# Kernel optimization log

Hardware: AMD Instinct MI355X
Metric: run time of the kernel (lower is better)

The kernel has to match this reference:

```python
import jax, jax.numpy as jnp
import numpy as np

N = 50000      # nodes
E = 800000     # edges (avg degree 16)
F_IN = 128     # in_channels
F_OUT = 64     # out_channels per head
H = 8          # attn heads
ALPHA = 0.2    # leaky relu slope


def setup_inputs() -> dict:
    key = jax.random.key(0)
    k1, k2, k3, k4, k5 = jax.random.split(key, 5)
    x = jax.random.normal(k1, (N, F_IN), dtype=jnp.float32)
    # guarantee every row appears as a source so rowsum > 0 (avoids NaN div)
    src = jnp.concatenate([jnp.arange(N, dtype=jnp.int32),
                           jax.random.randint(k2, (E - N,), 0, N, dtype=jnp.int32)])
    dst = jax.random.randint(k3, (E,), 0, N, dtype=jnp.int32)
    edge = jnp.stack([src, dst])  # [2, E]
    glorot = (6.0 / (F_IN + F_OUT)) ** 0.5
    W = jax.random.uniform(k4, (H, F_IN, F_OUT), jnp.float32, -glorot, glorot)
    a = jax.random.normal(k5, (H, 2 * F_OUT), dtype=jnp.float32) * 0.05
    return {"x": x, "edge": edge, "W": W, "a": a}


def reference(x, edge, W, a):
    # dropout p=0.6 treated in eval mode (identity); activation=None -> identity
    n = x.shape[0]
    src, dst = edge[0], edge[1]
    # per-head projected features: [H, N, F_OUT]
    h = jnp.einsum('nf,hfo->hno', x, W)
    a_src, a_dst = a[:, :F_OUT], a[:, F_OUT:]
    # edge scores a . cat(h_src, h_dst) decomposed into two node-level dots
    s = (jnp.einsum('hno,ho->hn', h, a_src)[:, src]
         + jnp.einsum('hno,ho->hn', h, a_dst)[:, dst])          # [H, E]
    edge_e = jnp.exp(-jax.nn.leaky_relu(s, ALPHA))               # [H, E]
    seg = lambda v: jax.ops.segment_sum(v, src, num_segments=n)
    rowsum = jax.vmap(seg)(edge_e)                               # [H, N] == spmm(e, ones)
    msg = edge_e[..., None] * h[:, dst, :]                       # [H, E, F_OUT]
    h_prime = jax.vmap(seg)(msg)                                 # [H, N, F_OUT]
    out = h_prime / rowsum[..., None]
    # concat heads: [N, H*F_OUT]
    return jnp.transpose(out, (1, 0, 2)).reshape(n, H * F_OUT)
```

## Files before the change

kernel.cpp:

```cpp
#include <hip/hip_runtime.h>
#include <hip/hip_bf16.h>
#include <math.h>

#define N_NODES 50000
#define N_EDGES 800000
#define FIN 128
#define FOUT 64
#define NH 8
#define ALPHA 0.2f
#define HSTRIDE (NH * FOUT)
#define SCAN_B 196

#define X2BF_B 3125
#define BPT_B  64
#define APERM_B 4
#define HIST_B 1563
#define PREP_B (X2BF_B + BPT_B + APERM_B + HIST_B)

typedef __attribute__((ext_vector_type(8))) short bf16x8;
typedef __attribute__((ext_vector_type(4))) float f32x4;

__device__ __forceinline__ unsigned pack_bf2(float lo, float hi) {
    __hip_bfloat162 b = __float22bfloat162_rn(make_float2(lo, hi));
    return *(unsigned*)&b;
}

__global__ __launch_bounds__(256) void gat_prep(const float* __restrict__ x,
                                                const float* __restrict__ W,
                                                const float* __restrict__ a,
                                                const int* __restrict__ src,
                                                unsigned* __restrict__ xbf,
                                                unsigned* __restrict__ bpt,
                                                float* __restrict__ aperm,
                                                int* __restrict__ deg) {
    const int b = blockIdx.x;
    const int t = threadIdx.x;

    if (b < X2BF_B) {
        const size_t tt = (size_t)b * 256 + t;
        const size_t i  = tt * 8;
        const float4 v0 = *(const float4*)(x + i);
        const float4 v1 = *(const float4*)(x + i + 4);
        uint4 o;
        o.x = pack_bf2(v0.x, v0.y);
        o.y = pack_bf2(v0.z, v0.w);
        o.z = pack_bf2(v1.x, v1.y);
        o.w = pack_bf2(v1.z, v1.w);
        *(uint4*)(xbf + tt * 4) = o;
    } else if (b < X2BF_B + BPT_B) {
        const int gt   = (b - X2BF_B) * 256 + t;
        const int dcol = gt >> 5;
        const int kq   = gt & 31;
        const int head = dcol & 7, col = dcol >> 3;
        const float* wp = W + (size_t)head * (FIN * FOUT) + (size_t)(kq * 4) * FOUT + col;
        uint2 pk;
        pk.x = pack_bf2(wp[0],        wp[FOUT]);
        pk.y = pack_bf2(wp[2 * FOUT], wp[3 * FOUT]);
        *(uint2*)(bpt + (size_t)dcol * (FIN / 2) + kq * 2) = pk;
    } else if (b < X2BF_B + BPT_B + APERM_B) {
        const int idx  = (b - X2BF_B - BPT_B) * 256 + t;
        const int tab  = idx >> 9;
        const int dcol = idx & 511;
        aperm[idx] = a[(dcol & 7) * (2 * FOUT) + tab * FOUT + (dcol >> 3)];
    } else {
        const int e = ((b - X2BF_B - BPT_B - APERM_B) * 256 + t) * 2;
        if (e + 1 < N_EDGES) {
            const int2 s2 = *(const int2*)(src + e);
            atomicAdd(&deg[s2.x], 1);
            atomicAdd(&deg[s2.y], 1);
        } else if (e < N_EDGES) {
            atomicAdd(&deg[src[e]], 1);
        }
    }
}

__global__ __launch_bounds__(256) void gat_proj(const unsigned short* __restrict__ xbf,
                                                const unsigned short* __restrict__ bpt,
                                                const float* __restrict__ aperm,
                                                unsigned short* __restrict__ h2,
                                                float* __restrict__ ssrc,
                                                float* __restrict__ sdst) {
    const int lane = threadIdx.x & 63;
    const int wid  = blockIdx.x * 4 + (threadIdx.x >> 6);
    const int m0   = wid * 32;
    const int l15  = lane & 15;
    const int g    = lane >> 4;

    bf16x8 xf[2][4];
#pragma unroll
    for (int nh = 0; nh < 2; ++nh) {
        int node = m0 + nh * 16 + l15;
        if (node > N_NODES - 1) node = N_NODES - 1;
        const unsigned short* p = xbf + (size_t)node * FIN + g * 8;
#pragma unroll
        for (int ks = 0; ks < 4; ++ks)
            xf[nh][ks] = *(const bf16x8*)(p + ks * 32);
    }

    float sc1[2][4], sc2[2][4];
#pragma unroll
    for (int nh = 0; nh < 2; ++nh)
#pragma unroll
        for (int r = 0; r < 4; ++r) { sc1[nh][r] = 0.f; sc2[nh][r] = 0.f; }

    for (int stp = 0; stp < 16; ++stp) {
        const int dc0 = stp * 32;
        f32x4 acc[2][2];
#pragma unroll
        for (int dh = 0; dh < 2; ++dh)
#pragma unroll
            for (int nh = 0; nh < 2; ++nh)
                acc[dh][nh] = (f32x4){0.f, 0.f, 0.f, 0.f};

#pragma unroll
        for (int dh = 0; dh < 2; ++dh) {
            const unsigned short* p = bpt + (size_t)(dc0 + dh * 16 + l15) * FIN + g * 8;
#pragma unroll
            for (int ks = 0; ks < 4; ++ks) {
                const bf16x8 af = *(const bf16x8*)(p + ks * 32);
                acc[dh][0] = __builtin_amdgcn_mfma_f32_16x16x32_bf16(af, xf[0][ks], acc[dh][0], 0, 0, 0);
                acc[dh][1] = __builtin_amdgcn_mfma_f32_16x16x32_bf16(af, xf[1][ks], acc[dh][1], 0, 0, 0);
            }
        }

#pragma unroll
        for (int dh = 0; dh < 2; ++dh) {
            const float4 ap1 = *(const float4*)&aperm[dc0 + dh * 16 + g * 4];
            const float4 ap2 = *(const float4*)&aperm[512 + dc0 + dh * 16 + g * 4];
#pragma unroll
            for (int nh = 0; nh < 2; ++nh) {
                sc1[nh][0] += acc[dh][nh][0] * ap1.x;  sc2[nh][0] += acc[dh][nh][0] * ap2.x;
                sc1[nh][1] += acc[dh][nh][1] * ap1.y;  sc2[nh][1] += acc[dh][nh][1] * ap2.y;
                sc1[nh][2] += acc[dh][nh][2] * ap1.z;  sc2[nh][2] += acc[dh][nh][2] * ap2.z;
                sc1[nh][3] += acc[dh][nh][3] * ap1.w;  sc2[nh][3] += acc[dh][nh][3] * ap2.w;
            }
        }

#pragma unroll
        for (int nh = 0; nh < 2; ++nh) {
            const int node = m0 + nh * 16 + l15;
            if (node < N_NODES) {
#pragma unroll
                for (int dh = 0; dh < 2; ++dh) {
                    const int dc = dc0 + dh * 16 + g * 4;
                    uint2 pk;
                    pk.x = pack_bf2(acc[dh][nh][0], acc[dh][nh][1]);
                    pk.y = pack_bf2(acc[dh][nh][2], acc[dh][nh][3]);
                    *(uint2*)((char*)h2 + ((size_t)node * HSTRIDE + dc) * 2) = pk;
                }
            }
        }
    }

#pragma unroll
    for (int nh = 0; nh < 2; ++nh) {
        const int node = m0 + nh * 16 + l15;
        float4 v1 = make_float4(sc1[nh][0], sc1[nh][1], sc1[nh][2], sc1[nh][3]);
        float4 v2 = make_float4(sc2[nh][0], sc2[nh][1], sc2[nh][2], sc2[nh][3]);
        v1.x += __shfl_xor(v1.x, 32, 64); v1.y += __shfl_xor(v1.y, 32, 64);
        v1.z += __shfl_xor(v1.z, 32, 64); v1.w += __shfl_xor(v1.w, 32, 64);
        v2.x += __shfl_xor(v2.x, 32, 64); v2.y += __shfl_xor(v2.y, 32, 64);
        v2.z += __shfl_xor(v2.z, 32, 64); v2.w += __shfl_xor(v2.w, 32, 64);
        if (node < N_NODES) {
            if (g == 0) { *(float4*)&ssrc[node * 8]     = v1; *(float4*)&sdst[node * 8]     = v2; }
            if (g == 1) { *(float4*)&ssrc[node * 8 + 4] = v1; *(float4*)&sdst[node * 8 + 4] = v2; }
        }
    }
}

__global__ __launch_bounds__(256) void scan_bsum(const int* __restrict__ deg,
                                                 int* __restrict__ bsum) {
    __shared__ int sm[256];
    const int t   = threadIdx.x;
    const int gid = blockIdx.x * 256 + t;
    sm[t] = (gid < N_NODES) ? deg[gid] : 0;
    __syncthreads();
#pragma unroll
    for (int off = 128; off > 0; off >>= 1) {
        if (t < off) sm[t] += sm[t + off];
        __syncthreads();
    }
    if (t == 0) bsum[blockIdx.x] = sm[0];
}

__global__ __launch_bounds__(256) void scan_part(int* __restrict__ bsum) {
    __shared__ int sm[256];
    const int t = threadIdx.x;
    const int v = (t < SCAN_B) ? bsum[t] : 0;
    sm[t] = v;
    __syncthreads();
    for (int off = 1; off < 256; off <<= 1) {
        const int u = (t >= off) ? sm[t - off] : 0;
        __syncthreads();
        sm[t] += u;
        __syncthreads();
    }
    if (t < SCAN_B) bsum[t] = sm[t] - v;
}

__global__ __launch_bounds__(256) void scan_write(const int* __restrict__ deg,
                                                  const int* __restrict__ bsum,
                                                  int* __restrict__ row_start,
                                                  int* __restrict__ cursor) {
    __shared__ int sm[256];
    const int t   = threadIdx.x;
    const int gid = blockIdx.x * 256 + t;
    const int v   = (gid < N_NODES) ? deg[gid] : 0;
    sm[t] = v;
    __syncthreads();
    for (int off = 1; off < 256; off <<= 1) {
        const int u = (t >= off) ? sm[t - off] : 0;
        __syncthreads();
        sm[t] += u;
        __syncthreads();
    }
    if (gid < N_NODES) {
        const int rs = bsum[blockIdx.x] + sm[t] - v;
        row_start[gid] = rs;
        cursor[gid]    = rs;
    }
    if (blockIdx.x == 0 && t == 0) row_start[N_NODES] = N_EDGES;
}

__global__ __launch_bounds__(256) void gat_fill(const int* __restrict__ src,
                                                const int* __restrict__ dst,
                                                int* __restrict__ cursor,
                                                int* __restrict__ csr_dst) {
    const int e = blockIdx.x * 256 + threadIdx.x;
    if (e >= N_EDGES) return;
    const int pos = atomicAdd(&cursor[src[e]], 1);
    csr_dst[pos] = dst[e];
}

#define GAT_LD(KK) (*(const uint4*)(h2b + ((size_t)(unsigned)__builtin_amdgcn_readlane(d, (KK)) << 10) + lofs))

#define GAT_FMA(HV, KK) do {                                                          \
    const float e0 = __int_as_float(__builtin_amdgcn_readlane(__float_as_int(e[0]), (KK))); \
    const float e1 = __int_as_float(__builtin_amdgcn_readlane(__float_as_int(e[1]), (KK))); \
    const float e2 = __int_as_float(__builtin_amdgcn_readlane(__float_as_int(e[2]), (KK))); \
    const float e3 = __int_as_float(__builtin_amdgcn_readlane(__float_as_int(e[3]), (KK))); \
    const float e4 = __int_as_float(__builtin_amdgcn_readlane(__float_as_int(e[4]), (KK))); \
    const float e5 = __int_as_float(__builtin_amdgcn_readlane(__float_as_int(e[5]), (KK))); \
    const float e6 = __int_as_float(__builtin_amdgcn_readlane(__float_as_int(e[6]), (KK))); \
    const float e7 = __int_as_float(__builtin_amdgcn_readlane(__float_as_int(e[7]), (KK))); \
    acc[0] += e0 * __int_as_float((HV).x << 16);                                      \
    acc[1] += e1 * __int_as_float((HV).x & 0xFFFF0000u);                              \
    acc[2] += e2 * __int_as_float((HV).y << 16);                                      \
    acc[3] += e3 * __int_as_float((HV).y & 0xFFFF0000u);                              \
    acc[4] += e4 * __int_as_float((HV).z << 16);                                      \
    acc[5] += e5 * __int_as_float((HV).z & 0xFFFF0000u);                              \
    acc[6] += e6 * __int_as_float((HV).w << 16);                                      \
    acc[7] += e7 * __int_as_float((HV).w & 0xFFFF0000u);                              \
} while (0)

__global__ __launch_bounds__(256) void gat_gather(const int* __restrict__ row_start,
                                                  const int* __restrict__ csr_dst,
                                                  const __hip_bfloat16* __restrict__ h2,
                                                  const float* __restrict__ ssrc,
                                                  const float* __restrict__ sdst,
                                                  float* __restrict__ out) {
    const int n    = (int)((blockIdx.x * 256 + threadIdx.x) >> 6);
    const int lane = threadIdx.x & 63;
    if (n >= N_NODES) return;

    const int start = row_start[n];
    const int degn  = row_start[n + 1] - start;

    const float4 sa = *(const float4*)(ssrc + n * 8);
    const float4 sb = *(const float4*)(ssrc + n * 8 + 4);
    const float s0[8] = {sa.x, sa.y, sa.z, sa.w, sb.x, sb.y, sb.z, sb.w};

    float acc[8] = {0.f, 0.f, 0.f, 0.f, 0.f, 0.f, 0.f, 0.f};
    float rs[8]  = {0.f, 0.f, 0.f, 0.f, 0.f, 0.f, 0.f, 0.f};
    const unsigned lofs = (unsigned)lane * 16u;
    const char* h2b = (const char*)h2;

    for (int base = 0; base < degn; base += 64) {
        const int j      = base + lane;
        const bool valid = j < degn;
        const int d = valid ? __builtin_nontemporal_load(csr_dst + start + j) : 0;
        float4 qa = make_float4(0.f, 0.f, 0.f, 0.f), qb = qa;
        if (valid) {
            qa = *(const float4*)(sdst + d * 8);
            qb = *(const float4*)(sdst + d * 8 + 4);
        }
        const float q[8] = {qa.x, qa.y, qa.z, qa.w, qb.x, qb.y, qb.z, qb.w};
        float e[8];
#pragma unroll
        for (int i = 0; i < 8; ++i) {
            const float sv = s0[i] + q[i];
            const float lr = sv > 0.f ? sv : ALPHA * sv;
            e[i] = valid ? __expf(-lr) : 0.f;
            rs[i] += e[i];
        }

        const int cnt = min(64, degn - base);
        int k = 0;
        if (cnt >= 8) {
            uint4 q0 = GAT_LD(0), q1 = GAT_LD(1), q2 = GAT_LD(2), q3 = GAT_LD(3);
            for (k = 0; k + 8 <= cnt; k += 4) {
                GAT_FMA(q0, k + 0); q0 = GAT_LD(k + 4);
                GAT_FMA(q1, k + 1); q1 = GAT_LD(k + 5);
                GAT_FMA(q2, k + 2); q2 = GAT_LD(k + 6);
                GAT_FMA(q3, k + 3); q3 = GAT_LD(k + 7);
            }
            GAT_FMA(q0, k + 0);
            GAT_FMA(q1, k + 1);
            GAT_FMA(q2, k + 2);
            GAT_FMA(q3, k + 3);
            k += 4;
        }
        for (; k < cnt; ++k) {
            const uint4 qv = GAT_LD(k);
            GAT_FMA(qv, k);
        }
    }

#pragma unroll
    for (int i = 0; i < 8; ++i)
#pragma unroll
        for (int m = 1; m < 64; m <<= 1) rs[i] += __shfl_xor(rs[i], m, 64);

#pragma unroll
    for (int i = 0; i < 8; ++i)
        __builtin_nontemporal_store(acc[i] / rs[i], &out[(size_t)n * HSTRIDE + i * 64 + lane]);
}

extern "C" void kernel_launch(void* const* d_in, const int* in_sizes, int n_in,
                              void* d_out, int out_size, void* d_ws, size_t ws_size,
                              hipStream_t stream) {
    const float* x    = (const float*)d_in[0];
    const int*   edge = (const int*)d_in[1];
    const float* W    = (const float*)d_in[2];
    const float* a    = (const float*)d_in[3];
    float*       out  = (float*)d_out;

    char* ws = (char*)d_ws;
    size_t off = 0;
    unsigned short* h2  = (unsigned short*)(ws + off); off += (size_t)N_NODES * HSTRIDE * 2;
    unsigned short* xbf = (unsigned short*)(ws + off); off += (size_t)N_NODES * FIN * 2;
    unsigned short* bpt = (unsigned short*)(ws + off); off += (size_t)HSTRIDE * FIN * 2;
    float* aperm  = (float*)(ws + off); off += (size_t)2 * HSTRIDE * sizeof(float);
    float* ssrc   = (float*)(ws + off); off += (size_t)N_NODES * NH * sizeof(float);
    float* sdst   = (float*)(ws + off); off += (size_t)N_NODES * NH * sizeof(float);
    int*   row_st = (int*)  (ws + off); off += (size_t)(N_NODES + 4) * sizeof(int);
    int*   cursor = (int*)  (ws + off); off += (size_t)N_NODES * sizeof(int);
    int*   deg    = (int*)  (ws + off); off += (size_t)N_NODES * sizeof(int);
    int*   bsum   = (int*)  (ws + off); off += (size_t)256 * sizeof(int);
    int*   csrd   = (int*)  (ws + off); off += (size_t)N_EDGES * sizeof(int);

    const int* srcv = edge;
    const int* dstv = edge + N_EDGES;

    hipMemsetAsync(deg, 0, (size_t)N_NODES * sizeof(int), stream);

    gat_prep  <<<PREP_B, 256, 0, stream>>>(x, W, a, srcv, (unsigned*)xbf, (unsigned*)bpt, aperm, deg);
    gat_proj  <<<(N_NODES + 127) / 128, 256, 0, stream>>>(xbf, bpt, aperm, h2, ssrc, sdst);
    scan_bsum <<<SCAN_B, 256, 0, stream>>>(deg, bsum);
    scan_part <<<1, 256, 0, stream>>>(bsum);
    scan_write<<<SCAN_B, 256, 0, stream>>>(deg, bsum, row_st, cursor);
    gat_fill  <<<(N_EDGES + 255) / 256, 256, 0, stream>>>(srcv, dstv, cursor, csrd);
    gat_gather<<<(N_NODES + 3) / 4, 256, 0, stream>>>(row_st, csrd, (const __hip_bfloat16*)h2, ssrc, sdst, out);
}
```

Before: 267.3 us.

## Fuse prep, degree histogram, scan and CSR fill into one cooperative kernel

Replaces the memset, the prep kernel, three scan kernels and the fill kernel with a single cooperative kernel on a persistent 512-block grid that uses grid.sync between phases. The goal is to remove the launch overhead and the inter-kernel gaps of the short CSR-build stages. In exchange it adds grid-wide barriers and a fixed grid size that may underuse the GPU during the bandwidth-bound x-to-bf16 conversion and atomic phases. Cooperative launch also requires that all 512 blocks be co-resident.

```diff
diff --git a/kernel.cpp b/kernel.cpp
--- a/kernel.cpp
+++ b/kernel.cpp
@@ -1,6 +1,9 @@
 #include <hip/hip_runtime.h>
 #include <hip/hip_bf16.h>
+#include <hip/hip_cooperative_groups.h>
 #include <math.h>
+
+namespace cg = cooperative_groups;
 
 #define N_NODES 50000
 #define N_EDGES 800000
@@ -10,12 +13,7 @@
 #define ALPHA 0.2f
 #define HSTRIDE (NH * FOUT)
 #define SCAN_B 196
-
-#define X2BF_B 3125
-#define BPT_B  64
-#define APERM_B 4
-#define HIST_B 1563
-#define PREP_B (X2BF_B + BPT_B + APERM_B + HIST_B)
+#define BUILD_GRID 512
 
 typedef __attribute__((ext_vector_type(8))) short bf16x8;
 typedef __attribute__((ext_vector_type(4))) float f32x4;
@@ -25,52 +23,114 @@
     return *(unsigned*)&b;
 }
 
-__global__ __launch_bounds__(256) void gat_prep(const float* __restrict__ x,
-                                                const float* __restrict__ W,
-                                                const float* __restrict__ a,
-                                                const int* __restrict__ src,
-                                                unsigned* __restrict__ xbf,
-                                                unsigned* __restrict__ bpt,
-                                                float* __restrict__ aperm,
-                                                int* __restrict__ deg) {
-    const int b = blockIdx.x;
-    const int t = threadIdx.x;
-
-    if (b < X2BF_B) {
-        const size_t tt = (size_t)b * 256 + t;
-        const size_t i  = tt * 8;
-        const float4 v0 = *(const float4*)(x + i);
-        const float4 v1 = *(const float4*)(x + i + 4);
+__global__ __launch_bounds__(256, 2) void gat_build(const float* __restrict__ x,
+                                                    const float* __restrict__ W,
+                                                    const float* __restrict__ a,
+                                                    const int* __restrict__ src,
+                                                    const int* __restrict__ dst,
+                                                    unsigned* __restrict__ xbf,
+                                                    unsigned* __restrict__ bpt,
+                                                    float* __restrict__ aperm,
+                                                    int* __restrict__ deg,
+                                                    int* __restrict__ bsum,
+                                                    int* __restrict__ row_start,
+                                                    int* __restrict__ cursor,
+                                                    int* __restrict__ csr_dst) {
+    cg::grid_group grid = cg::this_grid();
+    const int t   = threadIdx.x;
+    const int b   = blockIdx.x;
+    const int tid = b * 256 + t;
+    const int T   = BUILD_GRID * 256;
+
+    for (int i = tid; i < N_NODES * FIN / 8; i += T) {
+        const size_t ii = (size_t)i * 8;
+        const float4 v0 = *(const float4*)(x + ii);
+        const float4 v1 = *(const float4*)(x + ii + 4);
         uint4 o;
         o.x = pack_bf2(v0.x, v0.y);
         o.y = pack_bf2(v0.z, v0.w);
         o.z = pack_bf2(v1.x, v1.y);
         o.w = pack_bf2(v1.z, v1.w);
-        *(uint4*)(xbf + tt * 4) = o;
-    } else if (b < X2BF_B + BPT_B) {
-        const int gt   = (b - X2BF_B) * 256 + t;
-        const int dcol = gt >> 5;
-        const int kq   = gt & 31;
+        *(uint4*)(xbf + (size_t)i * 4) = o;
+    }
+    if (tid < HSTRIDE * 32) {
+        const int dcol = tid >> 5;
+        const int kq   = tid & 31;
         const int head = dcol & 7, col = dcol >> 3;
         const float* wp = W + (size_t)head * (FIN * FOUT) + (size_t)(kq * 4) * FOUT + col;
         uint2 pk;
         pk.x = pack_bf2(wp[0],        wp[FOUT]);
         pk.y = pack_bf2(wp[2 * FOUT], wp[3 * FOUT]);
         *(uint2*)(bpt + (size_t)dcol * (FIN / 2) + kq * 2) = pk;
-    } else if (b < X2BF_B + BPT_B + APERM_B) {
-        const int idx  = (b - X2BF_B - BPT_B) * 256 + t;
-        const int tab  = idx >> 9;
-        const int dcol = idx & 511;
-        aperm[idx] = a[(dcol & 7) * (2 * FOUT) + tab * FOUT + (dcol >> 3)];
-    } else {
-        const int e = ((b - X2BF_B - BPT_B - APERM_B) * 256 + t) * 2;
-        if (e + 1 < N_EDGES) {
-            const int2 s2 = *(const int2*)(src + e);
-            atomicAdd(&deg[s2.x], 1);
-            atomicAdd(&deg[s2.y], 1);
-        } else if (e < N_EDGES) {
-            atomicAdd(&deg[src[e]], 1);
-        }
+    }
+    if (tid < 2 * HSTRIDE) {
+        const int tab  = tid >> 9;
+        const int dcol = tid & 511;
+        aperm[tid] = a[(dcol & 7) * (2 * FOUT) + tab * FOUT + (dcol >> 3)];
+    }
+    for (int i = tid; i < N_NODES; i += T) deg[i] = 0;
+
+    grid.sync();
+
+    for (int i = tid; i < N_EDGES / 2; i += T) {
+        const int2 s2 = *(const int2*)(src + (size_t)i * 2);
+        atomicAdd(&deg[s2.x], 1);
+        atomicAdd(&deg[s2.y], 1);
+    }
+
+    grid.sync();
+
+    __shared__ int sm[256];
+    if (b < SCAN_B) {
+        const int gid = b * 256 + t;
+        sm[t] = (gid < N_NODES) ? deg[gid] : 0;
+        __syncthreads();
+#pragma unroll
+        for (int off = 128; off > 0; off >>= 1) {
+            if (t < off) sm[t] += sm[t + off];
+            __syncthreads();
+        }
+        if (t == 0) bsum[b] = sm[0];
+    }
+
+    grid.sync();
+
+    if (b < SCAN_B) {
+        __shared__ int smp[256];
+        const int pv = (t < SCAN_B) ? bsum[t] : 0;
+        smp[t] = pv;
+        __syncthreads();
+        for (int off = 1; off < 256; off <<= 1) {
+            const int u = (t >= off) ? smp[t - off] : 0;
+            __syncthreads();
+            smp[t] += u;
+            __syncthreads();
+        }
+        const int base = (b > 0) ? smp[b - 1] : 0;
+
+        const int gid = b * 256 + t;
+        const int v   = (gid < N_NODES) ? deg[gid] : 0;
+        sm[t] = v;
+        __syncthreads();
+        for (int off = 1; off < 256; off <<= 1) {
+            const int u = (t >= off) ? sm[t - off] : 0;
+            __syncthreads();
+            sm[t] += u;
+            __syncthreads();
+        }
+        if (gid < N_NODES) {
+            const int rs = base + sm[t] - v;
+            row_start[gid] = rs;
+            cursor[gid]    = rs;
+        }
+        if (b == 0 && t == 0) row_start[N_NODES] = N_EDGES;
+    }
+
+    grid.sync();
+
+    for (int i = tid; i < N_EDGES; i += T) {
+        const int pos = atomicAdd(&cursor[src[i]], 1);
+        csr_dst[pos] = dst[i];
     }
 }
 
@@ -166,70 +226,6 @@
             if (g == 1) { *(float4*)&ssrc[node * 8 + 4] = v1; *(float4*)&sdst[node * 8 + 4] = v2; }
         }
     }
-}
-
-__global__ __launch_bounds__(256) void scan_bsum(const int* __restrict__ deg,
-                                                 int* __restrict__ bsum) {
-    __shared__ int sm[256];
-    const int t   = threadIdx.x;
-    const int gid = blockIdx.x * 256 + t;
-    sm[t] = (gid < N_NODES) ? deg[gid] : 0;
-    __syncthreads();
-#pragma unroll
-    for (int off = 128; off > 0; off >>= 1) {
-        if (t < off) sm[t] += sm[t + off];
-        __syncthreads();
-    }
-    if (t == 0) bsum[blockIdx.x] = sm[0];
-}
-
-__global__ __launch_bounds__(256) void scan_part(int* __restrict__ bsum) {
-    __shared__ int sm[256];
-    const int t = threadIdx.x;
-    const int v = (t < SCAN_B) ? bsum[t] : 0;
-    sm[t] = v;
-    __syncthreads();
-    for (int off = 1; off < 256; off <<= 1) {
-        const int u = (t >= off) ? sm[t - off] : 0;
-        __syncthreads();
-        sm[t] += u;
-        __syncthreads();
-    }
-    if (t < SCAN_B) bsum[t] = sm[t] - v;
-}
-
-__global__ __launch_bounds__(256) void scan_write(const int* __restrict__ deg,
-                                                  const int* __restrict__ bsum,
-                                                  int* __restrict__ row_start,
-                                                  int* __restrict__ cursor) {
-    __shared__ int sm[256];
-    const int t   = threadIdx.x;
-    const int gid = blockIdx.x * 256 + t;
-    const int v   = (gid < N_NODES) ? deg[gid] : 0;
-    sm[t] = v;
-    __syncthreads();
-    for (int off = 1; off < 256; off <<= 1) {
-        const int u = (t >= off) ? sm[t - off] : 0;
-        __syncthreads();
-        sm[t] += u;
-        __syncthreads();
-    }
-    if (gid < N_NODES) {
-        const int rs = bsum[blockIdx.x] + sm[t] - v;
-        row_start[gid] = rs;
-        cursor[gid]    = rs;
-    }
-    if (blockIdx.x == 0 && t == 0) row_start[N_NODES] = N_EDGES;
-}
-
-__global__ __launch_bounds__(256) void gat_fill(const int* __restrict__ src,
-                                                const int* __restrict__ dst,
-                                                int* __restrict__ cursor,
-                                                int* __restrict__ csr_dst) {
-    const int e = blockIdx.x * 256 + threadIdx.x;
-    if (e >= N_EDGES) return;
-    const int pos = atomicAdd(&cursor[src[e]], 1);
-    csr_dst[pos] = dst[e];
 }
 
 #define GAT_LD(KK) (*(const uint4*)(h2b + ((size_t)(unsigned)__builtin_amdgcn_readlane(d, (KK)) << 10) + lofs))
@@ -352,13 +348,11 @@
     const int* srcv = edge;
     const int* dstv = edge + N_EDGES;
 
-    hipMemsetAsync(deg, 0, (size_t)N_NODES * sizeof(int), stream);
-
-    gat_prep  <<<PREP_B, 256, 0, stream>>>(x, W, a, srcv, (unsigned*)xbf, (unsigned*)bpt, aperm, deg);
+    void* bargs[] = {(void*)&x, (void*)&W, (void*)&a, (void*)&srcv, (void*)&dstv,
+                     (void*)&xbf, (void*)&bpt, (void*)&aperm, (void*)&deg,
+                     (void*)&bsum, (void*)&row_st, (void*)&cursor, (void*)&csrd};
+    hipLaunchCooperativeKernel((void*)gat_build, dim3(BUILD_GRID), dim3(256), bargs, 0, stream);
+
     gat_proj  <<<(N_NODES + 127) / 128, 256, 0, stream>>>(xbf, bpt, aperm, h2, ssrc, sdst);
-    scan_bsum <<<SCAN_B, 256, 0, stream>>>(deg, bsum);
-    scan_part <<<1, 256, 0, stream>>>(bsum);
-    scan_write<<<SCAN_B, 256, 0, stream>>>(deg, bsum, row_st, cursor);
-    gat_fill  <<<(N_EDGES + 255) / 256, 256, 0, stream>>>(srcv, dstv, cursor, csrd);
     gat_gather<<<(N_NODES + 3) / 4, 256, 0, stream>>>(row_st, csrd, (const __hip_bfloat16*)h2, ssrc, sdst, out);
 }
```

Result: slower. 524.5 us (+96.2%).

## Fuse x-to-bf16 conversion into projection and fold block-prefix scan into scan_write

Applied to the files above, without the earlier changes.

Removes the separate pass that converts x to a bf16 workspace copy; the projection kernel now loads fp32 x directly and packs it to bf16 in registers. The single-block scan_part kernel is dropped, and each scan_write block instead redundantly scans the 196 block sums in shared memory. The projection launch is moved after CSR construction. Together these cut one launch, one full intermediate write and read of x, and a serialized tiny kernel, at the cost of doubling the projection's x load bytes and repeating a small scan in every block.

```diff
diff --git a/kernel.cpp b/kernel.cpp
--- a/kernel.cpp
+++ b/kernel.cpp
@@ -11,11 +11,10 @@
 #define HSTRIDE (NH * FOUT)
 #define SCAN_B 196
 
-#define X2BF_B 3125
 #define BPT_B  64
 #define APERM_B 4
 #define HIST_B 1563
-#define PREP_B (X2BF_B + BPT_B + APERM_B + HIST_B)
+#define PREP_B (BPT_B + APERM_B + HIST_B)
 
 typedef __attribute__((ext_vector_type(8))) short bf16x8;
 typedef __attribute__((ext_vector_type(4))) float f32x4;
@@ -25,30 +24,17 @@
     return *(unsigned*)&b;
 }
 
-__global__ __launch_bounds__(256) void gat_prep(const float* __restrict__ x,
-                                                const float* __restrict__ W,
+__global__ __launch_bounds__(256) void gat_prep(const float* __restrict__ W,
                                                 const float* __restrict__ a,
                                                 const int* __restrict__ src,
-                                                unsigned* __restrict__ xbf,
                                                 unsigned* __restrict__ bpt,
                                                 float* __restrict__ aperm,
                                                 int* __restrict__ deg) {
     const int b = blockIdx.x;
     const int t = threadIdx.x;
 
-    if (b < X2BF_B) {
-        const size_t tt = (size_t)b * 256 + t;
-        const size_t i  = tt * 8;
-        const float4 v0 = *(const float4*)(x + i);
-        const float4 v1 = *(const float4*)(x + i + 4);
-        uint4 o;
-        o.x = pack_bf2(v0.x, v0.y);
-        o.y = pack_bf2(v0.z, v0.w);
-        o.z = pack_bf2(v1.x, v1.y);
-        o.w = pack_bf2(v1.z, v1.w);
-        *(uint4*)(xbf + tt * 4) = o;
-    } else if (b < X2BF_B + BPT_B) {
-        const int gt   = (b - X2BF_B) * 256 + t;
+    if (b < BPT_B) {
+        const int gt   = b * 256 + t;
         const int dcol = gt >> 5;
         const int kq   = gt & 31;
         const int head = dcol & 7, col = dcol >> 3;
@@ -57,13 +43,13 @@
         pk.x = pack_bf2(wp[0],        wp[FOUT]);
         pk.y = pack_bf2(wp[2 * FOUT], wp[3 * FOUT]);
         *(uint2*)(bpt + (size_t)dcol * (FIN / 2) + kq * 2) = pk;
-    } else if (b < X2BF_B + BPT_B + APERM_B) {
-        const int idx  = (b - X2BF_B - BPT_B) * 256 + t;
+    } else if (b < BPT_B + APERM_B) {
+        const int idx  = (b - BPT_B) * 256 + t;
         const int tab  = idx >> 9;
         const int dcol = idx & 511;
         aperm[idx] = a[(dcol & 7) * (2 * FOUT) + tab * FOUT + (dcol >> 3)];
     } else {
-        const int e = ((b - X2BF_B - BPT_B - APERM_B) * 256 + t) * 2;
+        const int e = ((b - BPT_B - APERM_B) * 256 + t) * 2;
         if (e + 1 < N_EDGES) {
             const int2 s2 = *(const int2*)(src + e);
             atomicAdd(&deg[s2.x], 1);
@@ -74,7 +60,7 @@
     }
 }
 
-__global__ __launch_bounds__(256) void gat_proj(const unsigned short* __restrict__ xbf,
+__global__ __launch_bounds__(256) void gat_proj(const float* __restrict__ x,
                                                 const unsigned short* __restrict__ bpt,
                                                 const float* __restrict__ aperm,
                                                 unsigned short* __restrict__ h2,
@@ -91,10 +77,17 @@
     for (int nh = 0; nh < 2; ++nh) {
         int node = m0 + nh * 16 + l15;
         if (node > N_NODES - 1) node = N_NODES - 1;
-        const unsigned short* p = xbf + (size_t)node * FIN + g * 8;
-#pragma unroll
-        for (int ks = 0; ks < 4; ++ks)
-            xf[nh][ks] = *(const bf16x8*)(p + ks * 32);
+        const float* p = x + (size_t)node * FIN + g * 8;
+#pragma unroll
+        for (int ks = 0; ks < 4; ++ks) {
+            const float4 a0 = *(const float4*)(p + ks * 32);
+            const float4 a1 = *(const float4*)(p + ks * 32 + 4);
+            unsigned* u = (unsigned*)&xf[nh][ks];
+            u[0] = pack_bf2(a0.x, a0.y);
+            u[1] = pack_bf2(a0.z, a0.w);
+            u[2] = pack_bf2(a1.x, a1.y);
+            u[3] = pack_bf2(a1.z, a1.w);
+        }
     }
 
     float sc1[2][4], sc2[2][4];
@@ -183,28 +176,27 @@
     if (t == 0) bsum[blockIdx.x] = sm[0];
 }
 
-__global__ __launch_bounds__(256) void scan_part(int* __restrict__ bsum) {
-    __shared__ int sm[256];
-    const int t = threadIdx.x;
-    const int v = (t < SCAN_B) ? bsum[t] : 0;
-    sm[t] = v;
-    __syncthreads();
-    for (int off = 1; off < 256; off <<= 1) {
-        const int u = (t >= off) ? sm[t - off] : 0;
-        __syncthreads();
-        sm[t] += u;
-        __syncthreads();
-    }
-    if (t < SCAN_B) bsum[t] = sm[t] - v;
-}
-
 __global__ __launch_bounds__(256) void scan_write(const int* __restrict__ deg,
                                                   const int* __restrict__ bsum,
                                                   int* __restrict__ row_start,
                                                   int* __restrict__ cursor) {
+    __shared__ int smp[256];
     __shared__ int sm[256];
-    const int t   = threadIdx.x;
-    const int gid = blockIdx.x * 256 + t;
+    const int t = threadIdx.x;
+    const int b = blockIdx.x;
+
+    const int pv = (t < SCAN_B) ? bsum[t] : 0;
+    smp[t] = pv;
+    __syncthreads();
+    for (int off = 1; off < 256; off <<= 1) {
+        const int u = (t >= off) ? smp[t - off] : 0;
+        __syncthreads();
+        smp[t] += u;
+        __syncthreads();
+    }
+    const int base = (b > 0) ? smp[b - 1] : 0;
+
+    const int gid = b * 256 + t;
     const int v   = (gid < N_NODES) ? deg[gid] : 0;
     sm[t] = v;
     __syncthreads();
@@ -215,11 +207,11 @@
         __syncthreads();
     }
     if (gid < N_NODES) {
-        const int rs = bsum[blockIdx.x] + sm[t] - v;
+        const int rs = base + sm[t] - v;
         row_start[gid] = rs;
         cursor[gid]    = rs;
     }
-    if (blockIdx.x == 0 && t == 0) row_start[N_NODES] = N_EDGES;
+    if (b == 0 && t == 0) row_start[N_NODES] = N_EDGES;
 }
 
 __global__ __launch_bounds__(256) void gat_fill(const int* __restrict__ src,
@@ -338,7 +330,6 @@
     char* ws = (char*)d_ws;
     size_t off = 0;
     unsigned short* h2  = (unsigned short*)(ws + off); off += (size_t)N_NODES * HSTRIDE * 2;
-    unsigned short* xbf = (unsigned short*)(ws + off); off += (size_t)N_NODES * FIN * 2;
     unsigned short* bpt = (unsigned short*)(ws + off); off += (size_t)HSTRIDE * FIN * 2;
     float* aperm  = (float*)(ws + off); off += (size_t)2 * HSTRIDE * sizeof(float);
     float* ssrc   = (float*)(ws + off); off += (size_t)N_NODES * NH * sizeof(float);
@@ -354,11 +345,10 @@
 
     hipMemsetAsync(deg, 0, (size_t)N_NODES * sizeof(int), stream);
 
-    gat_prep  <<<PREP_B, 256, 0, stream>>>(x, W, a, srcv, (unsigned*)xbf, (unsigned*)bpt, aperm, deg);
-    gat_proj  <<<(N_NODES + 127) / 128, 256, 0, stream>>>(xbf, bpt, aperm, h2, ssrc, sdst);
+    gat_prep  <<<PREP_B, 256, 0, stream>>>(W, a, srcv, (unsigned*)bpt, aperm, deg);
     scan_bsum <<<SCAN_B, 256, 0, stream>>>(deg, bsum);
-    scan_part <<<1, 256, 0, stream>>>(bsum);
     scan_write<<<SCAN_B, 256, 0, stream>>>(deg, bsum, row_st, cursor);
     gat_fill  <<<(N_EDGES + 255) / 256, 256, 0, stream>>>(srcv, dstv, cursor, csrd);
+    gat_proj  <<<(N_NODES + 127) / 128, 256, 0, stream>>>(x, bpt, aperm, h2, ssrc, sdst);
     gat_gather<<<(N_NODES + 3) / 4, 256, 0, stream>>>(row_st, csrd, (const __hip_bfloat16*)h2, ssrc, sdst, out);
 }
```

Measured after the change: 266.6 us. Within noise of the previous version (-0.3%).
